# Performance work log

Measured on AMD Instinct MI355X. Metric: run time of the kernel, lower is better.

The kernel has to match this reference:

```python
import jax, jax.numpy as jnp
import numpy as np
from jax.ops import segment_sum, segment_max

N = 100000   # nodes
E = 1000000  # edges
G = 100      # graphs in batch
NF, EF = 9, 2
FT, FE = 3, 8
HID = 64
H, C = 4, 16          # heads, per-head channels (H*C == HID, concat=True)
LAT = 32
L = 3                 # num GAT layers
NEG_SLOPE = 0.2       # PyG GATConv LeakyReLU slope


def setup_inputs() -> dict:
    key = jax.random.key(0)
    ks = jax.random.split(key, 20)
    def nrm(k, shp, s=0.05):
        return jax.random.normal(k, shp, jnp.float32) * s
    return dict(
        x=jax.random.normal(ks[0], (N, NF), jnp.float32),
        face_types=jax.random.randint(ks[1], (N,), 0, FT),
        edge_index=jax.random.randint(ks[2], (2, E), 0, N),
        edge_attr=jax.random.normal(ks[3], (E, EF), jnp.float32),
        batch=jnp.sort(jax.random.randint(ks[4], (N,), 0, G)),
        node_mask=jnp.ones((N,), jnp.float32),
        num_graphs=G,
        face_emb=nrm(ks[5], (FT, FE)),
        node_W=nrm(ks[6], (NF + FE, HID)), node_b=jnp.zeros((HID,), jnp.float32),
        edge_W=nrm(ks[7], (EF, HID)), edge_b=jnp.zeros((HID,), jnp.float32),
        gat_lin=nrm(ks[8], (L, HID, HID)),
        gat_lin_edge=nrm(ks[9], (L, HID, HID)),
        gat_att_src=nrm(ks[10], (L, H, C)),
        gat_att_dst=nrm(ks[11], (L, H, C)),
        gat_att_edge=nrm(ks[12], (L, H, C)),
        gat_bias=jnp.zeros((L, HID), jnp.float32),
        mu_W=nrm(ks[13], (HID, LAT)), mu_b=jnp.zeros((LAT,), jnp.float32),
        lv_W=nrm(ks[14], (HID, LAT)), lv_b=jnp.zeros((LAT,), jnp.float32),
    )


def _gat(h, src, dst, edge_h, W, We, a_s, a_d, a_e, b):
    """PyG GATConv (eval): shared lin, self-loops with fill_value='mean', segment softmax over dst."""
    n = h.shape[0]
    xh = (h @ W).reshape(n, H, C)                       # (N,H,C)
    al_s = (xh * a_s).sum(-1)                           # (N,H)
    al_d = (xh * a_d).sum(-1)                           # (N,H)
    # self-loop edge_attr = mean of incoming encoded edge features (fill_value='mean')
    deg = segment_sum(jnp.ones((src.shape[0],), h.dtype), dst, num_segments=n)
    loop_attr = segment_sum(edge_h, dst, num_segments=n) / jnp.clip(deg, 1.0)[:, None]
    loops = jnp.arange(n)
    sa = jnp.concatenate([src, loops])                  # (E+N,)
    da = jnp.concatenate([dst, loops])
    ea = jnp.concatenate([edge_h, loop_attr], axis=0)   # (E+N,HID)
    eh = (ea @ We).reshape(-1, H, C)
    al_e = (eh * a_e).sum(-1)                           # (E+N,H)
    alpha = jax.nn.leaky_relu(al_s[sa] + al_d[da] + al_e, NEG_SLOPE)
    amax = segment_max(alpha, da, num_segments=n)       # every node has a self-loop -> no empty segment
    ex = jnp.exp(alpha - amax[da])
    denom = segment_sum(ex, da, num_segments=n)
    w = ex / denom[da]                                  # (E+N,H)
    out = segment_sum(xh[sa] * w[:, :, None], da, num_segments=n)  # (N,H,C)
    return out.reshape(n, H * C) + b


def reference(x, face_types, edge_index, edge_attr, batch, node_mask, num_graphs,
              face_emb, node_W, node_b, edge_W, edge_b,
              gat_lin, gat_lin_edge, gat_att_src, gat_att_dst, gat_att_edge, gat_bias,
              mu_W, mu_b, lv_W, lv_b):
    h = jax.nn.relu(jnp.concatenate([x, face_emb[face_types]], axis=-1) @ node_W + node_b)
    edge_h = jax.nn.relu(edge_attr @ edge_W + edge_b)
    src, dst = edge_index[0], edge_index[1]
    for l in range(gat_lin.shape[0]):
        h = jax.nn.relu(_gat(h, src, dst, edge_h, gat_lin[l], gat_lin_edge[l],
                             gat_att_src[l], gat_att_dst[l], gat_att_edge[l], gat_bias[l]))
    # masked scatter-mean pooling per graph
    hm = h * node_mask[:, None]
    h_sum = segment_sum(hm, batch, num_segments=num_graphs)
    counts = segment_sum(node_mask, batch, num_segments=num_graphs)
    hp = h_sum / jnp.clip(counts, 1.0)[:, None]
    mu = hp @ mu_W + mu_b
    logvar = hp @ lv_W + lv_b
    return mu, logvar
```

## Files before the change

kernel.cpp:

```cpp
#include <hip/hip_runtime.h>
#include <math.h>

#define NN 100000
#define NE 1000000
#define NG 100
#define NL 3
#define NEG 0.2f

__device__ __forceinline__ float lrelu(float x){ return fmaxf(x, NEG*x); }

__global__ void k_ve(const float* __restrict__ We, const float* __restrict__ ae,
                     float* __restrict__ Ve2){
  int i = blockIdx.x*blockDim.x + threadIdx.x;
  if(i >= NL*4*64) return;
  int d = i & 63, h = (i>>6)&3, l = i>>8;
  const float* w = We + l*4096 + d*64 + h*16;
  const float* a = ae + l*64 + h*16;
  float s = 0.f;
  #pragma unroll
  for(int c=0;c<16;c++) s = fmaf(w[c], a[c], s);
  Ve2[(l*4+h)*64 + d] = s;
}

__global__ void k_h0(const float* __restrict__ x, const int* __restrict__ ft,
                     const float* __restrict__ femb, const float* __restrict__ W,
                     const float* __restrict__ b, float* __restrict__ h){
  int i = blockIdx.x*blockDim.x + threadIdx.x;
  if(i >= NN*64) return;
  int n = i>>6, d = i&63;
  const float* xr = x + (size_t)n*9;
  const float* fe = femb + ft[n]*8;
  float s = b[d];
  #pragma unroll
  for(int k=0;k<9;k++) s = fmaf(xr[k], W[k*64+d], s);
  #pragma unroll
  for(int j=0;j<8;j++) s = fmaf(fe[j], W[(9+j)*64+d], s);
  h[i] = fmaxf(s, 0.f);
}

__global__ void k_deg(const int* __restrict__ dst, int* __restrict__ deg){
  int i = blockIdx.x*blockDim.x + threadIdx.x;
  if(i >= NE/4) return;
  #pragma unroll
  for(int k=0;k<4;k++){
    int e = i + k*(NE/4);
    atomicAdd(&deg[dst[e]], 1);
  }
}

__global__ void k_scan1(const int* __restrict__ deg, int* __restrict__ rp,
                        int* __restrict__ bsum){
  __shared__ int sd[256];
  int t = threadIdx.x;
  int base = blockIdx.x*1024 + t*4;
  int v0 = (base+0<NN)?deg[base+0]:0;
  int v1 = (base+1<NN)?deg[base+1]:0;
  int v2 = (base+2<NN)?deg[base+2]:0;
  int v3 = (base+3<NN)?deg[base+3]:0;
  int ts = v0+v1+v2+v3;
  sd[t] = ts; __syncthreads();
  for(int off=1; off<256; off<<=1){
    int add = (t>=off)? sd[t-off] : 0;
    __syncthreads();
    sd[t] += add;
    __syncthreads();
  }
  int excl = sd[t] - ts;
  if(t==255) bsum[blockIdx.x] = sd[t];
  if(base+0<NN) rp[base+0]=excl;
  if(base+1<NN) rp[base+1]=excl+v0;
  if(base+2<NN) rp[base+2]=excl+v0+v1;
  if(base+3<NN) rp[base+3]=excl+v0+v1+v2;
}
__global__ void k_scan2(int* __restrict__ bsum, int nb){
  if(threadIdx.x==0 && blockIdx.x==0){
    int acc=0;
    for(int i=0;i<nb;i++){ int v=bsum[i]; bsum[i]=acc; acc+=v; }
  }
}
__global__ void k_scan3(int* __restrict__ rp, const int* __restrict__ bsum){
  int i = blockIdx.x*blockDim.x + threadIdx.x;
  if(i < NN) rp[i] += bsum[i>>10];
  if(i == 0) rp[NN] = NE;
}

__global__ void k_pack(const int* __restrict__ src, const float* __restrict__ eattr,
                       float4* __restrict__ pack){
  int e = blockIdx.x*blockDim.x + threadIdx.x;
  if(e >= NE) return;
  float4 r;
  r.x = __int_as_float(src[e]);
  r.y = eattr[(size_t)e*2];
  r.z = eattr[(size_t)e*2+1];
  r.w = 0.f;
  pack[e] = r;
}

__global__ void k_perm(const int* __restrict__ dst, const int* __restrict__ rp,
                       int* __restrict__ fill, int* __restrict__ perm){
  int i = blockIdx.x*blockDim.x + threadIdx.x;
  if(i >= NE/4) return;
  int e0 = i, e1 = i + (NE/4), e2 = i + 2*(NE/4), e3 = i + 3*(NE/4);
  int d0 = dst[e0], d1 = dst[e1], d2 = dst[e2], d3 = dst[e3];
  int p0 = rp[d0] + atomicAdd(&fill[d0], 1);
  int p1 = rp[d1] + atomicAdd(&fill[d1], 1);
  int p2 = rp[d2] + atomicAdd(&fill[d2], 1);
  int p3 = rp[d3] + atomicAdd(&fill[d3], 1);
  perm[p0] = e0;
  perm[p1] = e1;
  perm[p2] = e2;
  perm[p3] = e3;
}

__global__ void k_edge(const int* __restrict__ perm, const float4* __restrict__ pack,
                       const float* __restrict__ eW, const float* __restrict__ eb,
                       const float* __restrict__ Ve2,
                       int* __restrict__ csrc, float* __restrict__ cal){
  int e = blockIdx.x*blockDim.x + threadIdx.x;
  if(e >= NE) return;
  int eid = perm[e];
  float4 r = pack[eid];
  int ss = __float_as_int(r.x);
  float a0 = r.y, a1 = r.z;
  float acc[12];
  #pragma unroll
  for(int t=0;t<12;t++) acc[t]=0.f;
  #pragma unroll 4
  for(int d=0; d<64; d+=4){
    float4 w0 = *(const float4*)&eW[d];
    float4 w1 = *(const float4*)&eW[64+d];
    float4 bb = *(const float4*)&eb[d];
    float4 eh;
    eh.x = fmaxf(fmaf(a0, w0.x, fmaf(a1, w1.x, bb.x)), 0.f);
    eh.y = fmaxf(fmaf(a0, w0.y, fmaf(a1, w1.y, bb.y)), 0.f);
    eh.z = fmaxf(fmaf(a0, w0.z, fmaf(a1, w1.z, bb.z)), 0.f);
    eh.w = fmaxf(fmaf(a0, w0.w, fmaf(a1, w1.w, bb.w)), 0.f);
    #pragma unroll
    for(int j=0;j<12;j++){
      float4 v = *(const float4*)&Ve2[j*64 + d];
      acc[j] = fmaf(eh.x, v.x, acc[j]);
      acc[j] = fmaf(eh.y, v.y, acc[j]);
      acc[j] = fmaf(eh.z, v.z, acc[j]);
      acc[j] = fmaf(eh.w, v.w, acc[j]);
    }
  }
  csrc[e] = ss;
  *(float4*)&cal[(size_t)e*4]          = make_float4(acc[0], acc[1], acc[2],  acc[3]);
  *(float4*)&cal[((size_t)NE   + e)*4] = make_float4(acc[4], acc[5], acc[6],  acc[7]);
  *(float4*)&cal[((size_t)NE*2 + e)*4] = make_float4(acc[8], acc[9], acc[10], acc[11]);
}

__global__ __launch_bounds__(256) void k_xh(
    const float* __restrict__ hin, const float* __restrict__ W,
    const float* __restrict__ aS, const float* __restrict__ aD,
    float* __restrict__ xh, float* __restrict__ alsd){
  __shared__ float hs[64][68];
  __shared__ float Ws[64][64];
  int t  = threadIdx.x;
  int td = t & 15;
  int tn = t >> 4;
  int n0 = blockIdx.x*64;
  size_t base = (size_t)n0*64;
  #pragma unroll
  for(int i=0;i<4;i++){
    int idx4 = t + i*256;
    int row  = idx4 >> 4;
    int c4   = (idx4 & 15)*4;
    float4 hv = make_float4(0.f,0.f,0.f,0.f);
    if(base + (size_t)idx4*4 < (size_t)NN*64)
      hv = *(const float4*)&hin[base + (size_t)idx4*4];
    *(float4*)&hs[row][c4] = hv;
    *(float4*)&Ws[row][c4] = *(const float4*)&W[(size_t)idx4*4];
  }
  __syncthreads();

  float acc[4][4];
  #pragma unroll
  for(int i=0;i<4;i++)
    #pragma unroll
    for(int j=0;j<4;j++) acc[i][j]=0.f;

  for(int k=0;k<64;k+=4){
    float4 w0 = *(float4*)&Ws[k+0][td*4];
    float4 w1 = *(float4*)&Ws[k+1][td*4];
    float4 w2 = *(float4*)&Ws[k+2][td*4];
    float4 w3 = *(float4*)&Ws[k+3][td*4];
    #pragma unroll
    for(int i=0;i<4;i++){
      float4 hv = *(float4*)&hs[tn*4+i][k];
      acc[i][0] = fmaf(hv.x, w0.x, acc[i][0]);
      acc[i][1] = fmaf(hv.x, w0.y, acc[i][1]);
      acc[i][2] = fmaf(hv.x, w0.z, acc[i][2]);
      acc[i][3] = fmaf(hv.x, w0.w, acc[i][3]);
      acc[i][0] = fmaf(hv.y, w1.x, acc[i][0]);
      acc[i][1] = fmaf(hv.y, w1.y, acc[i][1]);
      acc[i][2] = fmaf(hv.y, w1.z, acc[i][2]);
      acc[i][3] = fmaf(hv.y, w1.w, acc[i][3]);
      acc[i][0] = fmaf(hv.z, w2.x, acc[i][0]);
      acc[i][1] = fmaf(hv.z, w2.y, acc[i][1]);
      acc[i][2] = fmaf(hv.z, w2.z, acc[i][2]);
      acc[i][3] = fmaf(hv.z, w2.w, acc[i][3]);
      acc[i][0] = fmaf(hv.w, w3.x, acc[i][0]);
      acc[i][1] = fmaf(hv.w, w3.y, acc[i][1]);
      acc[i][2] = fmaf(hv.w, w3.z, acc[i][2]);
      acc[i][3] = fmaf(hv.w, w3.w, acc[i][3]);
    }
  }

  float as0 = aS[td*4+0], as1 = aS[td*4+1], as2 = aS[td*4+2], as3 = aS[td*4+3];
  float ad0 = aD[td*4+0], ad1 = aD[td*4+1], ad2 = aD[td*4+2], ad3 = aD[td*4+3];
  int head = td>>2;

  #pragma unroll
  for(int i=0;i<4;i++){
    int n = n0 + tn*4 + i;
    if(n >= NN) break;
    *(float4*)&xh[(size_t)n*64 + td*4] =
        make_float4(acc[i][0], acc[i][1], acc[i][2], acc[i][3]);
    float vs = acc[i][0]*as0 + acc[i][1]*as1 + acc[i][2]*as2 + acc[i][3]*as3;
    float vd = acc[i][0]*ad0 + acc[i][1]*ad1 + acc[i][2]*ad2 + acc[i][3]*ad3;
    vs += __shfl_xor(vs, 1); vs += __shfl_xor(vs, 2);
    vd += __shfl_xor(vd, 1); vd += __shfl_xor(vd, 2);
    if((td&3)==0){
      alsd[(size_t)n*8 + head]     = vs;
      alsd[(size_t)n*8 + 4 + head] = vd;
    }
  }
}

__global__ __launch_bounds__(256) void k_gat(
    const float* __restrict__ xh, const float* __restrict__ alsd,
    const int* __restrict__ rp, const int* __restrict__ csrc,
    const float* __restrict__ cal, const float* __restrict__ bias,
    float* __restrict__ hout){
  int d = threadIdx.x & 63, h = d>>4;
  int n = __builtin_amdgcn_readfirstlane(blockIdx.x*4 + (threadIdx.x>>6));
  if(n >= NN) return;
  int r0 = rp[n], r1 = rp[n+1];
  int dg = r1 - r0;
  float alD_n = alsd[(size_t)n*8 + 4 + h];
  float m = -1e30f, den = 0.f, acc = 0.f, sum_al = 0.f;
  int p = r0;
  for(; p+8 <= r1; p += 8){
    int   s[8]; float e[8]; float a[8]; float x[8];
    #pragma unroll
    for(int k=0;k<8;k++) s[k] = csrc[p+k];
    #pragma unroll
    for(int k=0;k<8;k++) e[k] = cal[(size_t)(p+k)*4 + h];
    #pragma unroll
    for(int k=0;k<8;k++) a[k] = alsd[(size_t)s[k]*8 + h];
    #pragma unroll
    for(int k=0;k<8;k++) x[k] = xh[(size_t)s[k]*64 + d];
    float lg[8];
    float pmax = -1e30f;
    #pragma unroll
    for(int k=0;k<8;k++){
      sum_al += e[k];
      lg[k] = lrelu(a[k] + alD_n + e[k]);
      pmax = fmaxf(pmax, lg[k]);
    }
    if(pmax > m + 8.f){
      float sc = __expf(m - pmax);
      den *= sc; acc *= sc; m = pmax;
    }
    #pragma unroll
    for(int k=0;k<8;k++){
      float w = __expf(lg[k] - m);
      den += w;
      acc = fmaf(w, x[k], acc);
    }
  }
  for(; p < r1; p++){
    int s = csrc[p];
    float e = cal[(size_t)p*4 + h];
    float as = alsd[(size_t)s*8 + h];
    float xv = xh[(size_t)s*64 + d];
    sum_al += e;
    float lg = lrelu(as + alD_n + e);
    if(lg > m + 8.f){
      float sc = __expf(m - lg);
      den *= sc; acc *= sc; m = lg;
    }
    float w = __expf(lg - m); den += w; acc = fmaf(w, xv, acc);
  }
  float alS_n = alsd[(size_t)n*8 + h];
  float loop_al = dg>0 ? sum_al/(float)dg : 0.f;
  float la = lrelu(alS_n + alD_n + loop_al);
  float nm = fmaxf(m, la);
  float sc = __expf(m - nm);
  float wl = __expf(la - nm);
  den = den*sc + wl;
  acc = fmaf(wl, xh[(size_t)n*64+d], acc*sc);
  hout[(size_t)n*64+d] = fmaxf(acc/den + bias[d], 0.f);
}

__global__ void k_pool(const float* __restrict__ h, const int* __restrict__ batch,
                       const float* __restrict__ mask, float* __restrict__ hsum,
                       float* __restrict__ cnt){
  int d = threadIdx.x;
  int start = blockIdx.x*64;
  if(start >= NN) return;
  int end = min(start+64, NN);
  int curg = batch[start];
  float acc = 0.f, c = 0.f;
  for(int n=start; n<end; n++){
    int g = batch[n];
    if(g != curg){
      atomicAdd(&hsum[(size_t)curg*64+d], acc);
      if(d==0) atomicAdd(&cnt[curg], c);
      acc = 0.f; c = 0.f; curg = g;
    }
    float mk = mask[n];
    acc = fmaf(h[(size_t)n*64+d], mk, acc);
    if(d==0) c += mk;
  }
  atomicAdd(&hsum[(size_t)curg*64+d], acc);
  if(d==0) atomicAdd(&cnt[curg], c);
}

__global__ void k_final(const float* __restrict__ hsum, const float* __restrict__ cnt,
                        const float* __restrict__ muW, const float* __restrict__ mub,
                        const float* __restrict__ lvW, const float* __restrict__ lvb,
                        float* __restrict__ out){
  int i = blockIdx.x*blockDim.x + threadIdx.x;
  if(i >= NG*32*2) return;
  int which = i / (NG*32);
  int r = i % (NG*32);
  int g = r >> 5, j = r & 31;
  float rc = 1.f / fmaxf(cnt[g], 1.f);
  const float* W = which ? lvW : muW;
  float s = which ? lvb[j] : mub[j];
  const float* hr = hsum + (size_t)g*64;
  #pragma unroll 8
  for(int k=0;k<64;k++) s = fmaf(hr[k]*rc, W[k*32+j], s);
  out[i] = s;
}

extern "C" void kernel_launch(void* const* d_in, const int* in_sizes, int n_in,
                              void* d_out, int out_size, void* d_ws, size_t ws_size,
                              hipStream_t stream){
  const float* x      = (const float*)d_in[0];
  const int*   ft     = (const int*)d_in[1];
  const int*   ei     = (const int*)d_in[2];
  const float* eattr  = (const float*)d_in[3];
  const int*   batch  = (const int*)d_in[4];
  const float* mask   = (const float*)d_in[5];
  const float* femb   = (const float*)d_in[7];
  const float* nW     = (const float*)d_in[8];
  const float* nb     = (const float*)d_in[9];
  const float* eW     = (const float*)d_in[10];
  const float* ebias  = (const float*)d_in[11];
  const float* glin   = (const float*)d_in[12];
  const float* gline  = (const float*)d_in[13];
  const float* aS     = (const float*)d_in[14];
  const float* aD     = (const float*)d_in[15];
  const float* aE     = (const float*)d_in[16];
  const float* gbias  = (const float*)d_in[17];
  const float* muW    = (const float*)d_in[18];
  const float* mub    = (const float*)d_in[19];
  const float* lvW    = (const float*)d_in[20];
  const float* lvb    = (const float*)d_in[21];
  const int* src = ei;
  const int* dstp = ei + NE;

  char* ws = (char*)d_ws;
  size_t off = 0;
  auto alloc = [&](size_t bytes)->void*{
    void* p = ws + off; off += (bytes + 255) & ~(size_t)255; return p;
  };
  int*    deg   = (int*)   alloc((size_t)NN*4);
  int*    fill  = (int*)   alloc((size_t)NN*4);
  int*    rp    = (int*)   alloc((size_t)(NN+1)*4);
  int*    bsum  = (int*)   alloc(128*4);
  int*    perm  = (int*)   alloc((size_t)NE*4);
  float4* pack  = (float4*)alloc((size_t)NE*16);
  int*    csrc  = (int*)   alloc((size_t)NE*4);
  float*  cal   = (float*) alloc((size_t)NL*NE*4*4);
  float*  alsd  = (float*) alloc((size_t)NN*8*4);
  float*  Ve2   = (float*) alloc((size_t)NL*4*64*4);
  float*  hbuf  = (float*) alloc((size_t)NN*64*4);
  float*  xb    = (float*) alloc((size_t)NN*64*4);
  float*  hsum  = (float*) alloc((size_t)NG*64*4);
  float*  cnt   = (float*) alloc((size_t)NG*4);

  hipMemsetAsync(deg,  0, (size_t)NN*4, stream);
  hipMemsetAsync(fill, 0, (size_t)NN*4, stream);
  hipMemsetAsync(hsum, 0, (size_t)NG*64*4, stream);
  hipMemsetAsync(cnt,  0, (size_t)NG*4, stream);

  k_ve  <<<3, 256, 0, stream>>>(gline, aE, Ve2);
  k_h0  <<<(NN*64+255)/256, 256, 0, stream>>>(x, ft, femb, nW, nb, hbuf);
  k_deg <<<(NE/4+255)/256, 256, 0, stream>>>(dstp, deg);
  k_scan1<<<(NN+1023)/1024, 256, 0, stream>>>(deg, rp, bsum);
  k_scan2<<<1, 64, 0, stream>>>(bsum, (NN+1023)/1024);
  k_scan3<<<(NN+255)/256, 256, 0, stream>>>(rp, bsum);
  k_pack<<<(NE+255)/256, 256, 0, stream>>>(src, eattr, pack);
  k_perm<<<(NE/4+255)/256, 256, 0, stream>>>(dstp, rp, fill, perm);
  k_edge<<<(NE+255)/256, 256, 0, stream>>>(perm, pack, eW, ebias, Ve2, csrc, cal);

  for(int l=0;l<NL;l++){
    k_xh <<<(NN+63)/64, 256, 0, stream>>>(hbuf, glin + (size_t)l*4096,
                                          aS + l*64, aD + l*64, xb, alsd);
    k_gat<<<(NN+3)/4, 256, 0, stream>>>(xb, alsd, rp, csrc,
                                        cal + (size_t)l*NE*4, gbias + l*64, hbuf);
  }
  k_pool <<<(NN+63)/64, 64, 0, stream>>>(hbuf, batch, mask, hsum, cnt);
  k_final<<<(NG*32*2+255)/256, 256, 0, stream>>>(hsum, cnt, muW, mub, lvW, lvb,
                                                 (float*)d_out);
}
```

Measured before the change: 491.0 us.

## Build CSR via atomic rank, scatter edge records directly, pack per-edge data

The per-edge rank is captured from the degree atomic, so the separate pack and perm kernels and the fill atomics go away. The edge kernel now reads edges in original order and scatters a 64-byte record (source plus all three layers' edge logits) straight to its CSR slot. The GAT kernel reads source and edge logit from that interleaved record instead of separate csrc/cal arrays. The pooling kernel also moves to 256-thread blocks. The trade-off is scattered 64-byte writes and a strided gather in the GAT loop that only uses 8 of each 64 bytes per layer.

```diff
diff --git a/kernel.cpp b/kernel.cpp
--- a/kernel.cpp
+++ b/kernel.cpp
@@ -38,13 +38,14 @@
   h[i] = fmaxf(s, 0.f);
 }
 
-__global__ void k_deg(const int* __restrict__ dst, int* __restrict__ deg){
+__global__ void k_deg(const int* __restrict__ dst, int* __restrict__ deg,
+                      int* __restrict__ rank){
   int i = blockIdx.x*blockDim.x + threadIdx.x;
   if(i >= NE/4) return;
   #pragma unroll
   for(int k=0;k<4;k++){
     int e = i + k*(NE/4);
-    atomicAdd(&deg[dst[e]], 1);
+    rank[e] = atomicAdd(&deg[dst[e]], 1);
   }
 }
 
@@ -84,44 +85,14 @@
   if(i == 0) rp[NN] = NE;
 }
 
-__global__ void k_pack(const int* __restrict__ src, const float* __restrict__ eattr,
-                       float4* __restrict__ pack){
+__global__ void k_edge(const float* __restrict__ eattr, const int* __restrict__ src,
+                       const int* __restrict__ dst, const int* __restrict__ rank,
+                       const float* __restrict__ eW, const float* __restrict__ eb,
+                       const float* __restrict__ Ve2, const int* __restrict__ rp,
+                       float* __restrict__ rec){
   int e = blockIdx.x*blockDim.x + threadIdx.x;
   if(e >= NE) return;
-  float4 r;
-  r.x = __int_as_float(src[e]);
-  r.y = eattr[(size_t)e*2];
-  r.z = eattr[(size_t)e*2+1];
-  r.w = 0.f;
-  pack[e] = r;
-}
-
-__global__ void k_perm(const int* __restrict__ dst, const int* __restrict__ rp,
-                       int* __restrict__ fill, int* __restrict__ perm){
-  int i = blockIdx.x*blockDim.x + threadIdx.x;
-  if(i >= NE/4) return;
-  int e0 = i, e1 = i + (NE/4), e2 = i + 2*(NE/4), e3 = i + 3*(NE/4);
-  int d0 = dst[e0], d1 = dst[e1], d2 = dst[e2], d3 = dst[e3];
-  int p0 = rp[d0] + atomicAdd(&fill[d0], 1);
-  int p1 = rp[d1] + atomicAdd(&fill[d1], 1);
-  int p2 = rp[d2] + atomicAdd(&fill[d2], 1);
-  int p3 = rp[d3] + atomicAdd(&fill[d3], 1);
-  perm[p0] = e0;
-  perm[p1] = e1;
-  perm[p2] = e2;
-  perm[p3] = e3;
-}
-
-__global__ void k_edge(const int* __restrict__ perm, const float4* __restrict__ pack,
-                       const float* __restrict__ eW, const float* __restrict__ eb,
-                       const float* __restrict__ Ve2,
-                       int* __restrict__ csrc, float* __restrict__ cal){
-  int e = blockIdx.x*blockDim.x + threadIdx.x;
-  if(e >= NE) return;
-  int eid = perm[e];
-  float4 r = pack[eid];
-  int ss = __float_as_int(r.x);
-  float a0 = r.y, a1 = r.z;
+  float a0 = eattr[(size_t)e*2], a1 = eattr[(size_t)e*2+1];
   float acc[12];
   #pragma unroll
   for(int t=0;t<12;t++) acc[t]=0.f;
@@ -144,10 +115,13 @@
       acc[j] = fmaf(eh.w, v.w, acc[j]);
     }
   }
-  csrc[e] = ss;
-  *(float4*)&cal[(size_t)e*4]          = make_float4(acc[0], acc[1], acc[2],  acc[3]);
-  *(float4*)&cal[((size_t)NE   + e)*4] = make_float4(acc[4], acc[5], acc[6],  acc[7]);
-  *(float4*)&cal[((size_t)NE*2 + e)*4] = make_float4(acc[8], acc[9], acc[10], acc[11]);
+  int dd = dst[e];
+  int pos = rp[dd] + rank[e];
+  float* r = rec + (size_t)pos*16;
+  *(float4*)(r)    = make_float4(__int_as_float(src[e]), 0.f, 0.f, 0.f);
+  *(float4*)(r+4)  = make_float4(acc[0], acc[1], acc[2],  acc[3]);
+  *(float4*)(r+8)  = make_float4(acc[4], acc[5], acc[6],  acc[7]);
+  *(float4*)(r+12) = make_float4(acc[8], acc[9], acc[10], acc[11]);
 }
 
 __global__ __launch_bounds__(256) void k_xh(
@@ -230,23 +204,23 @@
 
 __global__ __launch_bounds__(256) void k_gat(
     const float* __restrict__ xh, const float* __restrict__ alsd,
-    const int* __restrict__ rp, const int* __restrict__ csrc,
-    const float* __restrict__ cal, const float* __restrict__ bias,
-    float* __restrict__ hout){
+    const int* __restrict__ rp, const float* __restrict__ rec,
+    int layer, const float* __restrict__ bias, float* __restrict__ hout){
   int d = threadIdx.x & 63, h = d>>4;
   int n = __builtin_amdgcn_readfirstlane(blockIdx.x*4 + (threadIdx.x>>6));
   if(n >= NN) return;
   int r0 = rp[n], r1 = rp[n+1];
   int dg = r1 - r0;
+  int loff = 4 + layer*4 + h;
   float alD_n = alsd[(size_t)n*8 + 4 + h];
   float m = -1e30f, den = 0.f, acc = 0.f, sum_al = 0.f;
   int p = r0;
   for(; p+8 <= r1; p += 8){
     int   s[8]; float e[8]; float a[8]; float x[8];
     #pragma unroll
-    for(int k=0;k<8;k++) s[k] = csrc[p+k];
-    #pragma unroll
-    for(int k=0;k<8;k++) e[k] = cal[(size_t)(p+k)*4 + h];
+    for(int k=0;k<8;k++) s[k] = ((const int*)rec)[(size_t)(p+k)*16];
+    #pragma unroll
+    for(int k=0;k<8;k++) e[k] = rec[(size_t)(p+k)*16 + loff];
     #pragma unroll
     for(int k=0;k<8;k++) a[k] = alsd[(size_t)s[k]*8 + h];
     #pragma unroll
@@ -271,8 +245,8 @@
     }
   }
   for(; p < r1; p++){
-    int s = csrc[p];
-    float e = cal[(size_t)p*4 + h];
+    int s = ((const int*)rec)[(size_t)p*16];
+    float e = rec[(size_t)p*16 + loff];
     float as = alsd[(size_t)s*8 + h];
     float xv = xh[(size_t)s*64 + d];
     sum_al += e;
@@ -294,11 +268,12 @@
   hout[(size_t)n*64+d] = fmaxf(acc/den + bias[d], 0.f);
 }
 
-__global__ void k_pool(const float* __restrict__ h, const int* __restrict__ batch,
-                       const float* __restrict__ mask, float* __restrict__ hsum,
-                       float* __restrict__ cnt){
-  int d = threadIdx.x;
-  int start = blockIdx.x*64;
+__global__ __launch_bounds__(256) void k_pool(
+    const float* __restrict__ h, const int* __restrict__ batch,
+    const float* __restrict__ mask, float* __restrict__ hsum,
+    float* __restrict__ cnt){
+  int d = threadIdx.x & 63;
+  int start = blockIdx.x*256 + (threadIdx.x>>6)*64;
   if(start >= NN) return;
   int end = min(start+64, NN);
   int curg = batch[start];
@@ -369,13 +344,10 @@
     void* p = ws + off; off += (bytes + 255) & ~(size_t)255; return p;
   };
   int*    deg   = (int*)   alloc((size_t)NN*4);
-  int*    fill  = (int*)   alloc((size_t)NN*4);
+  int*    rank  = (int*)   alloc((size_t)NE*4);
   int*    rp    = (int*)   alloc((size_t)(NN+1)*4);
   int*    bsum  = (int*)   alloc(128*4);
-  int*    perm  = (int*)   alloc((size_t)NE*4);
-  float4* pack  = (float4*)alloc((size_t)NE*16);
-  int*    csrc  = (int*)   alloc((size_t)NE*4);
-  float*  cal   = (float*) alloc((size_t)NL*NE*4*4);
+  float*  rec   = (float*) alloc((size_t)NE*16*4);
   float*  alsd  = (float*) alloc((size_t)NN*8*4);
   float*  Ve2   = (float*) alloc((size_t)NL*4*64*4);
   float*  hbuf  = (float*) alloc((size_t)NN*64*4);
@@ -384,27 +356,25 @@
   float*  cnt   = (float*) alloc((size_t)NG*4);
 
   hipMemsetAsync(deg,  0, (size_t)NN*4, stream);
-  hipMemsetAsync(fill, 0, (size_t)NN*4, stream);
   hipMemsetAsync(hsum, 0, (size_t)NG*64*4, stream);
   hipMemsetAsync(cnt,  0, (size_t)NG*4, stream);
 
   k_ve  <<<3, 256, 0, stream>>>(gline, aE, Ve2);
   k_h0  <<<(NN*64+255)/256, 256, 0, stream>>>(x, ft, femb, nW, nb, hbuf);
-  k_deg <<<(NE/4+255)/256, 256, 0, stream>>>(dstp, deg);
+  k_deg <<<(NE/4+255)/256, 256, 0, stream>>>(dstp, deg, rank);
   k_scan1<<<(NN+1023)/1024, 256, 0, stream>>>(deg, rp, bsum);
   k_scan2<<<1, 64, 0, stream>>>(bsum, (NN+1023)/1024);
   k_scan3<<<(NN+255)/256, 256, 0, stream>>>(rp, bsum);
-  k_pack<<<(NE+255)/256, 256, 0, stream>>>(src, eattr, pack);
-  k_perm<<<(NE/4+255)/256, 256, 0, stream>>>(dstp, rp, fill, perm);
-  k_edge<<<(NE+255)/256, 256, 0, stream>>>(perm, pack, eW, ebias, Ve2, csrc, cal);
+  k_edge<<<(NE+255)/256, 256, 0, stream>>>(eattr, src, dstp, rank, eW, ebias,
+                                           Ve2, rp, rec);
 
   for(int l=0;l<NL;l++){
     k_xh <<<(NN+63)/64, 256, 0, stream>>>(hbuf, glin + (size_t)l*4096,
                                           aS + l*64, aD + l*64, xb, alsd);
-    k_gat<<<(NN+3)/4, 256, 0, stream>>>(xb, alsd, rp, csrc,
-                                        cal + (size_t)l*NE*4, gbias + l*64, hbuf);
-  }
-  k_pool <<<(NN+63)/64, 64, 0, stream>>>(hbuf, batch, mask, hsum, cnt);
+    k_gat<<<(NN+3)/4, 256, 0, stream>>>(xb, alsd, rp, rec, l,
+                                        gbias + l*64, hbuf);
+  }
+  k_pool <<<(NN+255)/256, 256, 0, stream>>>(hbuf, batch, mask, hsum, cnt);
   k_final<<<(NG*32*2+255)/256, 256, 0, stream>>>(hsum, cnt, muW, mub, lvW, lvb,
                                                  (float*)d_out);
 }
```

Result: slower. 510.3 us (+3.9%).
